# Kernel tuning notes

Measured on AMD Instinct MI355X. Metric: run time of the kernel, lower is better.

## Reference

```python
import jax, jax.numpy as jnp
import numpy as np

BS, SEQ, NPL = 1024, 200, 22
HID = 128          # hidden_dim / rnn_dim
RNN_H = 2 * HID    # LSTMCell hidden = 256
ENC_D = HID // 2   # per-team set-encoder output = 64
IN_D = 2 * ENC_D + 44 + 3  # 175 = coords_encoded(128) + flat player trace(44) + closest_dist(1) + prev pred(2)
OUT_D = 2 + 88     # 'ball' target


def setup_inputs() -> dict:
    key = jax.random.key(0)
    ks = jax.random.split(key, 8)
    s = jnp.float32(0.02)
    return {
        "coords": jax.random.uniform(ks[0], (BS, SEQ, NPL * 4), dtype=jnp.float32),
        "pitch_size": jnp.ones((2,), jnp.float32),
        "W_e1": jax.random.normal(ks[1], (2, ENC_D), jnp.float32) * s,
        "b_e1": jnp.zeros((ENC_D,), jnp.float32),
        "W_e2": jax.random.normal(ks[2], (ENC_D, ENC_D), jnp.float32) * s,
        "b_e2": jnp.zeros((ENC_D,), jnp.float32),
        "W_ih": jax.random.normal(ks[3], (IN_D, 4 * RNN_H), jnp.float32) * s,
        "b_ih": jnp.zeros((4 * RNN_H,), jnp.float32),
        "W_hh": jax.random.normal(ks[4], (RNN_H, 4 * RNN_H), jnp.float32) * s,
        "b_hh": jnp.zeros((4 * RNN_H,), jnp.float32),
        "W_out": jax.random.normal(ks[5], (RNN_H, OUT_D), jnp.float32) * s,
        "b_out": jnp.zeros((OUT_D,), jnp.float32),
    }


def reference(coords, pitch_size, W_e1, b_e1, W_e2, b_e2,
              W_ih, b_ih, W_hh, b_hh, W_out, b_out):
    bs, seq_len, _ = coords.shape

    # per-team set encoder (DeepSets stand-in for SetTransformer(in=2, out=rnn_dim//2))
    pts = coords.reshape(bs, seq_len, NPL, 4)[..., :2]          # [bs, seq, 22, 2]
    def enc(t):                                                 # [bs, seq, 11, 2] -> [bs, seq, 64]
        h = jax.nn.relu(t @ W_e1 + b_e1)
        return h.mean(axis=2) @ W_e2 + b_e2
    coords_enc = jnp.concatenate(
        [enc(pts[:, :, :NPL // 2]), enc(pts[:, :, NPL // 2:])], axis=-1)  # [bs, seq, 128]

    # strided gathers: player_x = coords[..., 0:88:4], player_y = coords[..., 1:88:4]
    ptrace = jnp.stack([coords[:, :, 0:88:4], coords[:, :, 1:88:4]], axis=-1)  # [bs, seq, 22, 2]

    scale = jnp.tile(pitch_size, 45)                            # pitch_size.repeat(45) -> [90]

    def step(carry, xs):
        hx, cx, pred = carry                                    # pred = previous step_out[:, -2:]
        ptr_t, enc_t = xs                                       # [bs,22,2], [bs,128]
        dists = jnp.linalg.norm(pred[:, None, :] - ptr_t, axis=-1)   # [bs, 22]
        closest = jnp.min(dists, axis=-1, keepdims=True)             # [bs, 1]
        rnn_in = jnp.concatenate(
            [ptr_t.reshape(bs, -1), enc_t, closest, pred], axis=-1)  # [bs, 175]
        gates = rnn_in @ W_ih + b_ih + hx @ W_hh + b_hh              # [bs, 1024]
        i, f, g, o = jnp.split(gates, 4, axis=-1)
        cx2 = jax.nn.sigmoid(f) * cx + jax.nn.sigmoid(i) * jnp.tanh(g)
        hx2 = jax.nn.sigmoid(o) * jnp.tanh(cx2)
        step_out = (hx2 @ W_out + b_out) * scale                     # [bs, 90]
        return (hx2, cx2, step_out[:, -2:]), step_out

    init = (jnp.zeros((bs, RNN_H), coords.dtype),
            jnp.zeros((bs, RNN_H), coords.dtype),
            jnp.zeros((bs, 2), coords.dtype))
    xs = (ptrace.transpose(1, 0, 2, 3), coords_enc.transpose(1, 0, 2))
    _, outs = jax.lax.scan(step, init, xs)                      # [seq, bs, 90]
    return outs.transpose(1, 0, 2)                              # [bs, seq, 90]
```

## Files before the change

### kernel.cpp

```cpp
#include <hip/hip_runtime.h>
#include <math.h>

#define SEQ 200

typedef float f32x4 __attribute__((ext_vector_type(4)));
typedef short bf16x8 __attribute__((ext_vector_type(8)));

__device__ __forceinline__ float sigmoidf_(float x) { return 1.0f / (1.0f + __expf(-x)); }

__device__ __forceinline__ unsigned short bf16_rn(float v) {
    unsigned x = __float_as_uint(v);
    unsigned r = x + 0x7FFFu + ((x >> 16) & 1u);
    return (unsigned short)(r >> 16);
}
__device__ __forceinline__ float bf16_to_f(unsigned short h) {
    return __uint_as_float(((unsigned)h) << 16);
}
__device__ __forceinline__ void cvt_hl(float v, unsigned short& h, unsigned short& l) {
    h = bf16_rn(v);
    l = bf16_rn(v - bf16_to_f(h));
}

__global__ void prep_wt(const float* __restrict__ W_ih, const float* __restrict__ W_hh,
                        unsigned short* __restrict__ Wt_h, unsigned short* __restrict__ Wt_l) {
    int rc = blockIdx.x;
    int hj = rc >> 7, lc = rc & 127;
    int gcol = (lc >> 5) * 256 + hj * 32 + (lc & 31);
    for (int k = threadIdx.x; k < 448; k += 256) {
        float v = 0.f;
        if (k < 175) v = W_ih[(size_t)k * 1024 + gcol];
        else if (k >= 176 && k < 432) v = W_hh[(size_t)(k - 176) * 1024 + gcol];
        unsigned short h, l; cvt_hl(v, h, l);
        Wt_h[(size_t)rc * 448 + k] = h;
        Wt_l[(size_t)rc * 448 + k] = l;
    }
}

__global__ void prep_wo(const float* __restrict__ W_out,
                        unsigned short* __restrict__ Wt_oh, unsigned short* __restrict__ Wt_ol) {
    int rc = blockIdx.x;
    int hj = rc >> 4, c = rc & 15;
    int col = (c < 12) ? (hj * 12 + c) : (c < 14 ? 76 + c : 999);
    for (int k = threadIdx.x; k < 256; k += 256) {
        float v = (col < 90) ? W_out[(size_t)k * 90 + col] : 0.f;
        unsigned short h, l; cvt_hl(v, h, l);
        Wt_oh[(size_t)rc * 256 + k] = h;
        Wt_ol[(size_t)rc * 256 + k] = l;
    }
}

__global__ __launch_bounds__(256, 3) void enc_kernel(
    const float* __restrict__ coords,
    const float* __restrict__ W_e1, const float* __restrict__ b_e1,
    const float* __restrict__ W_e2, const float* __restrict__ b_e2,
    unsigned short* __restrict__ xin_h)
{
    __shared__ float C[32][45];
    __shared__ float H[32][2][65];
    __shared__ float W2[64][64];
    __shared__ unsigned short O16[128][34];

    int t  = blockIdx.x >> 5;
    int bc = blockIdx.x & 31;
    int tid = threadIdx.x;

    for (int idx = tid; idx < 32 * 44; idx += 256) {
        int bl = idx / 44, j = idx - bl * 44;
        C[bl][j] = coords[((size_t)(bc * 32 + bl) * SEQ + t) * 88 + (j >> 1) * 4 + (j & 1)];
    }
    for (int idx = tid; idx < 64 * 64; idx += 256)
        W2[idx >> 6][idx & 63] = W_e2[idx];
    __syncthreads();

    {
        int b  = tid >> 3;
        int cq = (tid & 7) * 8;
        float w0[8], w1[8], bb[8];
#pragma unroll
        for (int c = 0; c < 8; c++) { w0[c] = W_e1[cq + c]; w1[c] = W_e1[64 + cq + c]; bb[c] = b_e1[cq + c]; }
        for (int tm = 0; tm < 2; tm++) {
            float acc[8];
#pragma unroll
            for (int c = 0; c < 8; c++) acc[c] = 0.f;
            for (int p = 0; p < 11; p++) {
                float x = C[b][tm * 22 + p * 2];
                float y = C[b][tm * 22 + p * 2 + 1];
#pragma unroll
                for (int c = 0; c < 8; c++) {
                    float h = fmaf(x, w0[c], fmaf(y, w1[c], bb[c]));
                    acc[c] += fmaxf(h, 0.f);
                }
            }
#pragma unroll
            for (int c = 0; c < 8; c++) H[b][tm][cq + c] = acc[c] * (1.0f / 11.0f);
        }
    }
    __syncthreads();

    {
        int b  = tid >> 3;
        int tm = (tid >> 2) & 1;
        int ch = (tid & 3) * 16;
        float acc[16];
#pragma unroll
        for (int c = 0; c < 16; c++) acc[c] = 0.f;
        for (int k = 0; k < 64; k++) {
            float h = H[b][tm][k];
#pragma unroll
            for (int c = 0; c < 16; c++) acc[c] = fmaf(h, W2[k][ch + c], acc[c]);
        }
#pragma unroll
        for (int c = 0; c < 16; c++)
            O16[tm * 64 + ch + c][b] = bf16_rn(acc[c] + b_e2[ch + c]);
    }
    __syncthreads();

    unsigned short* xrow = xin_h + ((size_t)t * 1024 + bc * 32) * 176;
    for (int idx = tid; idx < 32 * 22; idx += 256) {
        int bl = idx / 22, oct = idx - bl * 22;
        unsigned short hs[8];
#pragma unroll
        for (int e = 0; e < 8; e++) {
            int k = oct * 8 + e;
            if (k < 44)       hs[e] = bf16_rn(C[bl][k]);
            else if (k < 172) hs[e] = O16[k - 44][bl];
            else              hs[e] = 0;
        }
        uint4 pk;
        pk.x = (unsigned)hs[0] | ((unsigned)hs[1] << 16);
        pk.y = (unsigned)hs[2] | ((unsigned)hs[3] << 16);
        pk.z = (unsigned)hs[4] | ((unsigned)hs[5] << 16);
        pk.w = (unsigned)hs[6] | ((unsigned)hs[7] << 16);
        *(uint4*)(xrow + (size_t)bl * 176 + oct * 8) = pk;
    }
}

#define MFMA_B(d, a, b) d = __builtin_amdgcn_mfma_f32_16x16x32_bf16(a, b, d, 0, 0, 0)

#define P_LOAD(R0, R1, R2, R3, KO) \
    R0 = *(const uint4*)(wbh + (size_t)c0 * 448 + (KO) + oct * 8); \
    R1 = *(const uint4*)(wbl + (size_t)c0 * 448 + (KO) + oct * 8); \
    R2 = *(const uint4*)(wbh + (size_t)c1 * 448 + (KO) + oct * 8); \
    R3 = *(const uint4*)(wbl + (size_t)c1 * 448 + (KO) + oct * 8);

#define P_STORE(R0, R1, R2, R3, NB) \
    *(uint4*)&BB[NB][0][c0 * 40 + oct * 8] = R0; \
    *(uint4*)&BB[NB][1][c0 * 40 + oct * 8] = R1; \
    *(uint4*)&BB[NB][0][c1 * 40 + oct * 8] = R2; \
    *(uint4*)&BB[NB][1][c1 * 40 + oct * 8] = R3;

__global__ __launch_bounds__(512, 1) void step_kernel(
    int t,
    const unsigned short* __restrict__ xin_h,
    const unsigned short* __restrict__ hxh_in, const unsigned short* __restrict__ hxl_in,
    unsigned short* __restrict__ hxh_out, unsigned short* __restrict__ hxl_out,
    float* __restrict__ cx,
    const unsigned short* __restrict__ Wt_h, const unsigned short* __restrict__ Wt_l,
    const unsigned short* __restrict__ Wt_oh, const unsigned short* __restrict__ Wt_ol,
    const float* __restrict__ b_ih, const float* __restrict__ b_hh,
    const float* __restrict__ b_out,
    const float* __restrict__ pitch, float* __restrict__ d_out)
{
    __shared__ unsigned short AH[32 * 456];
    __shared__ unsigned short AL[32 * 456];
    __shared__ unsigned short BB[3][2][128 * 40];
    __shared__ float U[128 * 33];
    __shared__ float predL[32][2];

    int tid = threadIdx.x;
    int bi = blockIdx.x & 31, hj = blockIdx.x >> 5;
    int bg0 = bi * 32;
    int l = tid & 63, w = (tid >> 6) & 3;
    int lr = l & 15, qa = l >> 4;

    const unsigned short* wbh = Wt_h + (size_t)(hj * 128) * 448;
    const unsigned short* wbl = Wt_l + (size_t)(hj * 128) * 448;

    for (int idx = tid; idx < 32 * 32; idx += 512) {
        int b = idx >> 5, oct = idx & 31;
        *(uint4*)&AH[b * 456 + 176 + oct * 8] =
            *(const uint4*)(hxh_in + (size_t)(bg0 + b) * 256 + oct * 8);
        *(uint4*)&AL[b * 456 + 176 + oct * 8] =
            *(const uint4*)(hxl_in + (size_t)(bg0 + b) * 256 + oct * 8);
    }
    if (t < SEQ) {
        const unsigned short* xr = xin_h + ((size_t)t * 1024 + bg0) * 176;
        for (int idx = tid; idx < 32 * 22; idx += 512) {
            int b = idx / 22, oct = idx - b * 22;
            *(uint4*)&AH[b * 456 + oct * 8] = *(const uint4*)(xr + (size_t)b * 176 + oct * 8);
        }
        if (tid < 64) {
            int b = tid >> 1, h8 = (tid & 1) * 8;
            *(uint4*)&AL[b * 456 + 160 + h8] = make_uint4(0, 0, 0, 0);
            *(uint4*)&AH[b * 456 + 432 + h8] = make_uint4(0, 0, 0, 0);
            *(uint4*)&AL[b * 456 + 432 + h8] = make_uint4(0, 0, 0, 0);
        }
        {
            int c = tid >> 2, o = tid & 3;
            *(uint4*)&BB[0][0][c * 40 + o * 8] = *(const uint4*)(wbh + (size_t)c * 448 + o * 8);
            *(uint4*)&BB[0][1][c * 40 + o * 8] = *(const uint4*)(wbl + (size_t)c * 448 + o * 8);
        }
    }
    __syncthreads();

    uint4 rA0, rA1, rA2, rA3, rB0, rB1, rB2, rB3;
    int c0 = (tid & 255) >> 2, oct = tid & 3, c1 = ((tid & 255) >> 2) + 64;
    if (tid < 256) {
        const unsigned short* woh = Wt_oh + ((size_t)(hj * 16 + lr)) * 256 + w * 64 + qa * 8;
        const unsigned short* wol = Wt_ol + ((size_t)(hj * 16 + lr)) * 256 + w * 64 + qa * 8;
        bf16x8 bh0 = *(const bf16x8*)(woh);
        bf16x8 bl0 = *(const bf16x8*)(wol);
        bf16x8 bh1 = *(const bf16x8*)(woh + 32);
        bf16x8 bl1 = *(const bf16x8*)(wol + 32);
        f32x4 acce[2];
        acce[0] = (f32x4){0.f, 0.f, 0.f, 0.f};
        acce[1] = (f32x4){0.f, 0.f, 0.f, 0.f};
#pragma unroll
        for (int ks2 = 0; ks2 < 2; ks2++) {
            bf16x8 bh = ks2 ? bh1 : bh0;
            bf16x8 bl = ks2 ? bl1 : bl0;
#pragma unroll
            for (int mt = 0; mt < 2; mt++) {
                bf16x8 ah = *(const bf16x8*)&AH[(mt * 16 + lr) * 456 + 176 + w * 64 + ks2 * 32 + qa * 8];
                bf16x8 al = *(const bf16x8*)&AL[(mt * 16 + lr) * 456 + 176 + w * 64 + ks2 * 32 + qa * 8];
                MFMA_B(acce[mt], ah, bh);
                MFMA_B(acce[mt], ah, bl);
                MFMA_B(acce[mt], al, bh);
            }
        }
#pragma unroll
        for (int mt = 0; mt < 2; mt++)
#pragma unroll
            for (int r = 0; r < 4; r++)
                U[w * 512 + (mt * 16 + qa * 4 + r) * 16 + lr] = acce[mt][r];
    } else if (t < SEQ) {
        P_LOAD(rA0, rA1, rA2, rA3, 32)
        P_LOAD(rB0, rB1, rB2, rB3, 64)
    }
    __syncthreads();

    if (tid < 256) {
#pragma unroll
        for (int j = 0; j < 2; j++) {
            int i = tid * 2 + j;
            int b = i >> 4, c = i & 15;
            float v = U[i] + U[512 + i] + U[1024 + i] + U[1536 + i];
            if (c < 14) {
                int col = (c < 12) ? (hj * 12 + c) : (76 + c);
                if (col < 90) {
                    if (t > 0) {
                        float vv = (v + b_out[col]) * pitch[c & 1];
                        if (c < 12) d_out[((size_t)(bg0 + b) * SEQ + (t - 1)) * 90 + col] = vv;
                        else predL[b][c - 12] = vv;
                    } else if (c >= 12) {
                        predL[b][c - 12] = 0.f;
                    }
                }
            }
        }
    }
    __syncthreads();

    if (t < SEQ) {
        if (tid < 32) {
            int b = tid;
            float p0 = predL[b][0], p1 = predL[b][1];
            float m = 1e30f;
#pragma unroll
            for (int p = 0; p < 22; p++) {
                float px = bf16_to_f(AH[b * 456 + 2 * p]);
                float py = bf16_to_f(AH[b * 456 + 2 * p + 1]);
                float dx = p0 - px, dy = p1 - py;
                m = fminf(m, fmaf(dx, dx, dy * dy));
            }
            unsigned short h, lo;
            cvt_hl(sqrtf(m), h, lo); AH[b * 456 + 172] = h; AL[b * 456 + 172] = lo;
            cvt_hl(p0, h, lo);       AH[b * 456 + 173] = h; AL[b * 456 + 173] = lo;
            cvt_hl(p1, h, lo);       AH[b * 456 + 174] = h; AL[b * 456 + 174] = lo;
        }
        __syncthreads();

        if (tid < 256) {
            f32x4 acc[2][2];
#pragma unroll
            for (int ct = 0; ct < 2; ct++)
#pragma unroll
                for (int mt = 0; mt < 2; mt++) acc[ct][mt] = (f32x4){0.f, 0.f, 0.f, 0.f};

#pragma unroll
            for (int ks = 0; ks < 14; ks++) {
                const int cur = ks % 3;
                bf16x8 ah[2], al[2], bh[2], bl[2];
#pragma unroll
                for (int mt = 0; mt < 2; mt++)
                    ah[mt] = *(const bf16x8*)&AH[(mt * 16 + lr) * 456 + ks * 32 + qa * 8];
                if (ks >= 5) {
#pragma unroll
                    for (int mt = 0; mt < 2; mt++)
                        al[mt] = *(const bf16x8*)&AL[(mt * 16 + lr) * 456 + ks * 32 + qa * 8];
                }
#pragma unroll
                for (int ct = 0; ct < 2; ct++) {
                    bh[ct] = *(const bf16x8*)&BB[cur][0][(w * 32 + ct * 16 + lr) * 40 + qa * 8];
                    bl[ct] = *(const bf16x8*)&BB[cur][1][(w * 32 + ct * 16 + lr) * 40 + qa * 8];
                }
#pragma unroll
                for (int ct = 0; ct < 2; ct++)
#pragma unroll
                    for (int mt = 0; mt < 2; mt++) {
                        MFMA_B(acc[ct][mt], ah[mt], bh[ct]);
                        MFMA_B(acc[ct][mt], ah[mt], bl[ct]);
                        if (ks >= 5) MFMA_B(acc[ct][mt], al[mt], bh[ct]);
                    }
                __syncthreads();
            }

#pragma unroll
            for (int ct = 0; ct < 2; ct++)
#pragma unroll
                for (int mt = 0; mt < 2; mt++)
#pragma unroll
                    for (int r = 0; r < 4; r++)
                        U[(w * 32 + ct * 16 + lr) * 33 + (mt * 16 + qa * 4 + r)] = acc[ct][mt][r];
        } else {
#pragma unroll
            for (int ks = 0; ks < 14; ks++) {
                if (ks <= 12) {
                    const int nb = (ks + 1) % 3;
                    if ((ks & 1) == 0) { P_STORE(rA0, rA1, rA2, rA3, nb) }
                    else               { P_STORE(rB0, rB1, rB2, rB3, nb) }
                }
                if (ks <= 10) {
                    const int ko = (ks + 3) * 32;
                    if ((ks & 1) == 0) { P_LOAD(rA0, rA1, rA2, rA3, ko) }
                    else               { P_LOAD(rB0, rB1, rB2, rB3, ko) }
                }
                __syncthreads();
            }
        }
        __syncthreads();

        if (tid < 256) {
            int b = tid & 31, hq = tid >> 5;
            unsigned short hh[4], hl[4];
#pragma unroll
            for (int q = 0; q < 4; q++) {
                int hlc = hq * 4 + q;
                int gb = hj * 32 + hlc;
                float iv = U[(0 * 32 + hlc) * 33 + b] + b_ih[gb]        + b_hh[gb];
                float fv = U[(1 * 32 + hlc) * 33 + b] + b_ih[256 + gb]  + b_hh[256 + gb];
                float gv = U[(2 * 32 + hlc) * 33 + b] + b_ih[512 + gb]  + b_hh[512 + gb];
                float ov = U[(3 * 32 + hlc) * 33 + b] + b_ih[768 + gb]  + b_hh[768 + gb];
                size_t cidx = (size_t)gb * 1024 + bg0 + b;
                float c_old = cx[cidx];
                float c_new = fmaf(sigmoidf_(fv), c_old, sigmoidf_(iv) * tanhf(gv));
                cx[cidx] = c_new;
                float hv = sigmoidf_(ov) * tanhf(c_new);
                cvt_hl(hv, hh[q], hl[q]);
            }
            size_t ho = (size_t)(bg0 + b) * 256 + hj * 32 + hq * 4;
            *(ushort4*)&hxh_out[ho] = make_ushort4(hh[0], hh[1], hh[2], hh[3]);
            *(ushort4*)&hxl_out[ho] = make_ushort4(hl[0], hl[1], hl[2], hl[3]);
        }
    }
}

extern "C" void kernel_launch(void* const* d_in, const int* in_sizes, int n_in,
                              void* d_out, int out_size, void* d_ws, size_t ws_size,
                              hipStream_t stream) {
    const float* coords = (const float*)d_in[0];
    const float* pitch  = (const float*)d_in[1];
    const float* W_e1   = (const float*)d_in[2];
    const float* b_e1   = (const float*)d_in[3];
    const float* W_e2   = (const float*)d_in[4];
    const float* b_e2   = (const float*)d_in[5];
    const float* W_ih   = (const float*)d_in[6];
    const float* b_ih   = (const float*)d_in[7];
    const float* W_hh   = (const float*)d_in[8];
    const float* b_hh   = (const float*)d_in[9];
    const float* W_out  = (const float*)d_in[10];
    const float* b_out  = (const float*)d_in[11];
    float* out = (float*)d_out;
    float* ws  = (float*)d_ws;

    float* cxb = ws;
    unsigned short* hxhA = (unsigned short*)(ws + 262144);
    unsigned short* hxlA = (unsigned short*)(ws + 393216);
    unsigned short* hxhB = (unsigned short*)(ws + 524288);
    unsigned short* hxlB = (unsigned short*)(ws + 655360);
    unsigned short* Wt_h = (unsigned short*)(ws + 786432);
    unsigned short* Wt_l = (unsigned short*)(ws + 1015808);
    unsigned short* Wt_oh = (unsigned short*)(ws + 1245184);
    unsigned short* Wt_ol = (unsigned short*)(ws + 1261568);
    unsigned short* xin_h = (unsigned short*)(ws + 1277952);

    hipMemsetAsync(ws, 0, (size_t)524288 * sizeof(float), stream);

    prep_wt<<<1024, 256, 0, stream>>>(W_ih, W_hh, Wt_h, Wt_l);
    prep_wo<<<128, 256, 0, stream>>>(W_out, Wt_oh, Wt_ol);
    enc_kernel<<<SEQ * 32, 256, 0, stream>>>(coords, W_e1, b_e1, W_e2, b_e2, xin_h);

    for (int t = 0; t <= SEQ; t++) {
        bool even = !(t & 1);
        step_kernel<<<256, 512, 0, stream>>>(
            t, xin_h,
            even ? hxhA : hxhB, even ? hxlA : hxlB,
            even ? hxhB : hxhA, even ? hxlB : hxlA,
            cxb, Wt_h, Wt_l, Wt_oh, Wt_ol, b_ih, b_hh, b_out, pitch, out);
    }
}
```

Baseline: 2.380 ms.

## Split step kernel into 512 smaller blocks reading weights directly from global

Each step block now covers 16 hidden units (64 gate columns) instead of 32, so the grid doubles to 512 blocks of 256 threads and every thread does MFMA work. The producer/consumer LDS triple-buffering of weight tiles is removed; MFMA B operands are loaded straight from global memory, relying on L2/cache. The output projection split is adjusted to 6 columns per block. This trades the LDS weight pipeline and the extra synchronisation it needed for more parallelism across the GPU's compute units. The cost is more redundant loading of the A (input/hidden) tile across blocks and global-latency-bound B loads.

New measurement: 2.800 ms. 1.18x slower.

```diff
diff --git a/kernel.cpp b/kernel.cpp
--- a/kernel.cpp
+++ b/kernel.cpp
@@ -24,8 +24,8 @@
 __global__ void prep_wt(const float* __restrict__ W_ih, const float* __restrict__ W_hh,
                         unsigned short* __restrict__ Wt_h, unsigned short* __restrict__ Wt_l) {
     int rc = blockIdx.x;
-    int hj = rc >> 7, lc = rc & 127;
-    int gcol = (lc >> 5) * 256 + hj * 32 + (lc & 31);
+    int hj = rc >> 6, lc = rc & 63;
+    int gcol = (lc >> 4) * 256 + hj * 16 + (lc & 15);
     for (int k = threadIdx.x; k < 448; k += 256) {
         float v = 0.f;
         if (k < 175) v = W_ih[(size_t)k * 1024 + gcol];
@@ -40,7 +40,7 @@
                         unsigned short* __restrict__ Wt_oh, unsigned short* __restrict__ Wt_ol) {
     int rc = blockIdx.x;
     int hj = rc >> 4, c = rc & 15;
-    int col = (c < 12) ? (hj * 12 + c) : (c < 14 ? 76 + c : 999);
+    int col = (c < 6) ? (hj * 6 + c) : (c < 8 ? 82 + c : 999);
     for (int k = threadIdx.x; k < 256; k += 256) {
         float v = (col < 90) ? W_out[(size_t)k * 90 + col] : 0.f;
         unsigned short h, l; cvt_hl(v, h, l);
@@ -137,19 +137,7 @@
 
 #define MFMA_B(d, a, b) d = __builtin_amdgcn_mfma_f32_16x16x32_bf16(a, b, d, 0, 0, 0)
 
-#define P_LOAD(R0, R1, R2, R3, KO) \
-    R0 = *(const uint4*)(wbh + (size_t)c0 * 448 + (KO) + oct * 8); \
-    R1 = *(const uint4*)(wbl + (size_t)c0 * 448 + (KO) + oct * 8); \
-    R2 = *(const uint4*)(wbh + (size_t)c1 * 448 + (KO) + oct * 8); \
-    R3 = *(const uint4*)(wbl + (size_t)c1 * 448 + (KO) + oct * 8);
-
-#define P_STORE(R0, R1, R2, R3, NB) \
-    *(uint4*)&BB[NB][0][c0 * 40 + oct * 8] = R0; \
-    *(uint4*)&BB[NB][1][c0 * 40 + oct * 8] = R1; \
-    *(uint4*)&BB[NB][0][c1 * 40 + oct * 8] = R2; \
-    *(uint4*)&BB[NB][1][c1 * 40 + oct * 8] = R3;
-
-__global__ __launch_bounds__(512, 1) void step_kernel(
+__global__ __launch_bounds__(256, 2) void step_kernel(
     int t,
     const unsigned short* __restrict__ xin_h,
     const unsigned short* __restrict__ hxh_in, const unsigned short* __restrict__ hxl_in,
@@ -163,20 +151,19 @@
 {
     __shared__ unsigned short AH[32 * 456];
     __shared__ unsigned short AL[32 * 456];
-    __shared__ unsigned short BB[3][2][128 * 40];
-    __shared__ float U[128 * 33];
+    __shared__ float U[2112];
     __shared__ float predL[32][2];
 
     int tid = threadIdx.x;
     int bi = blockIdx.x & 31, hj = blockIdx.x >> 5;
     int bg0 = bi * 32;
-    int l = tid & 63, w = (tid >> 6) & 3;
+    int l = tid & 63, w = tid >> 6;
     int lr = l & 15, qa = l >> 4;
 
-    const unsigned short* wbh = Wt_h + (size_t)(hj * 128) * 448;
-    const unsigned short* wbl = Wt_l + (size_t)(hj * 128) * 448;
-
-    for (int idx = tid; idx < 32 * 32; idx += 512) {
+    const unsigned short* wbh = Wt_h + (size_t)(hj * 64) * 448;
+    const unsigned short* wbl = Wt_l + (size_t)(hj * 64) * 448;
+
+    for (int idx = tid; idx < 32 * 32; idx += 256) {
         int b = idx >> 5, oct = idx & 31;
         *(uint4*)&AH[b * 456 + 176 + oct * 8] =
             *(const uint4*)(hxh_in + (size_t)(bg0 + b) * 256 + oct * 8);
@@ -185,7 +172,7 @@
     }
     if (t < SEQ) {
         const unsigned short* xr = xin_h + ((size_t)t * 1024 + bg0) * 176;
-        for (int idx = tid; idx < 32 * 22; idx += 512) {
+        for (int idx = tid; idx < 32 * 22; idx += 256) {
             int b = idx / 22, oct = idx - b * 22;
             *(uint4*)&AH[b * 456 + oct * 8] = *(const uint4*)(xr + (size_t)b * 176 + oct * 8);
         }
@@ -195,17 +182,10 @@
             *(uint4*)&AH[b * 456 + 432 + h8] = make_uint4(0, 0, 0, 0);
             *(uint4*)&AL[b * 456 + 432 + h8] = make_uint4(0, 0, 0, 0);
         }
-        {
-            int c = tid >> 2, o = tid & 3;
-            *(uint4*)&BB[0][0][c * 40 + o * 8] = *(const uint4*)(wbh + (size_t)c * 448 + o * 8);
-            *(uint4*)&BB[0][1][c * 40 + o * 8] = *(const uint4*)(wbl + (size_t)c * 448 + o * 8);
-        }
-    }
-    __syncthreads();
-
-    uint4 rA0, rA1, rA2, rA3, rB0, rB1, rB2, rB3;
-    int c0 = (tid & 255) >> 2, oct = tid & 3, c1 = ((tid & 255) >> 2) + 64;
-    if (tid < 256) {
+    }
+    __syncthreads();
+
+    {
         const unsigned short* woh = Wt_oh + ((size_t)(hj * 16 + lr)) * 256 + w * 64 + qa * 8;
         const unsigned short* wol = Wt_ol + ((size_t)(hj * 16 + lr)) * 256 + w * 64 + qa * 8;
         bf16x8 bh0 = *(const bf16x8*)(woh);
@@ -233,28 +213,21 @@
 #pragma unroll
             for (int r = 0; r < 4; r++)
                 U[w * 512 + (mt * 16 + qa * 4 + r) * 16 + lr] = acce[mt][r];
-    } else if (t < SEQ) {
-        P_LOAD(rA0, rA1, rA2, rA3, 32)
-        P_LOAD(rB0, rB1, rB2, rB3, 64)
-    }
-    __syncthreads();
-
-    if (tid < 256) {
-#pragma unroll
-        for (int j = 0; j < 2; j++) {
-            int i = tid * 2 + j;
-            int b = i >> 4, c = i & 15;
-            float v = U[i] + U[512 + i] + U[1024 + i] + U[1536 + i];
-            if (c < 14) {
-                int col = (c < 12) ? (hj * 12 + c) : (76 + c);
-                if (col < 90) {
-                    if (t > 0) {
-                        float vv = (v + b_out[col]) * pitch[c & 1];
-                        if (c < 12) d_out[((size_t)(bg0 + b) * SEQ + (t - 1)) * 90 + col] = vv;
-                        else predL[b][c - 12] = vv;
-                    } else if (c >= 12) {
-                        predL[b][c - 12] = 0.f;
-                    }
+    }
+    __syncthreads();
+
+    for (int idx = tid; idx < 512; idx += 256) {
+        int b = idx >> 4, c = idx & 15;
+        float v = U[idx] + U[512 + idx] + U[1024 + idx] + U[1536 + idx];
+        if (c < 8) {
+            int col = (c < 6) ? (hj * 6 + c) : (82 + c);
+            if (col < 90) {
+                if (t > 0) {
+                    float vv = (v + b_out[col]) * pitch[c & 1];
+                    if (c < 6) d_out[((size_t)(bg0 + b) * SEQ + (t - 1)) * 90 + col] = vv;
+                    else predL[b][c - 6] = vv;
+                } else if (c >= 6) {
+                    predL[b][c - 6] = 0.f;
                 }
             }
         }
@@ -280,87 +253,56 @@
         }
         __syncthreads();
 
-        if (tid < 256) {
-            f32x4 acc[2][2];
-#pragma unroll
-            for (int ct = 0; ct < 2; ct++)
-#pragma unroll
-                for (int mt = 0; mt < 2; mt++) acc[ct][mt] = (f32x4){0.f, 0.f, 0.f, 0.f};
-
+        {
+            f32x4 acc[2];
+            acc[0] = (f32x4){0.f, 0.f, 0.f, 0.f};
+            acc[1] = (f32x4){0.f, 0.f, 0.f, 0.f};
 #pragma unroll
             for (int ks = 0; ks < 14; ks++) {
-                const int cur = ks % 3;
-                bf16x8 ah[2], al[2], bh[2], bl[2];
-#pragma unroll
-                for (int mt = 0; mt < 2; mt++)
-                    ah[mt] = *(const bf16x8*)&AH[(mt * 16 + lr) * 456 + ks * 32 + qa * 8];
+                bf16x8 ah0 = *(const bf16x8*)&AH[(lr) * 456 + ks * 32 + qa * 8];
+                bf16x8 ah1 = *(const bf16x8*)&AH[(16 + lr) * 456 + ks * 32 + qa * 8];
+                bf16x8 bh = *(const bf16x8*)(wbh + (size_t)(w * 16 + lr) * 448 + ks * 32 + qa * 8);
+                bf16x8 bl = *(const bf16x8*)(wbl + (size_t)(w * 16 + lr) * 448 + ks * 32 + qa * 8);
+                MFMA_B(acc[0], ah0, bh);
+                MFMA_B(acc[0], ah0, bl);
+                MFMA_B(acc[1], ah1, bh);
+                MFMA_B(acc[1], ah1, bl);
                 if (ks >= 5) {
-#pragma unroll
-                    for (int mt = 0; mt < 2; mt++)
-                        al[mt] = *(const bf16x8*)&AL[(mt * 16 + lr) * 456 + ks * 32 + qa * 8];
+                    bf16x8 al0 = *(const bf16x8*)&AL[(lr) * 456 + ks * 32 + qa * 8];
+                    bf16x8 al1 = *(const bf16x8*)&AL[(16 + lr) * 456 + ks * 32 + qa * 8];
+                    MFMA_B(acc[0], al0, bh);
+                    MFMA_B(acc[1], al1, bh);
                 }
-#pragma unroll
-                for (int ct = 0; ct < 2; ct++) {
-                    bh[ct] = *(const bf16x8*)&BB[cur][0][(w * 32 + ct * 16 + lr) * 40 + qa * 8];
-                    bl[ct] = *(const bf16x8*)&BB[cur][1][(w * 32 + ct * 16 + lr) * 40 + qa * 8];
-                }
-#pragma unroll
-                for (int ct = 0; ct < 2; ct++)
-#pragma unroll
-                    for (int mt = 0; mt < 2; mt++) {
-                        MFMA_B(acc[ct][mt], ah[mt], bh[ct]);
-                        MFMA_B(acc[ct][mt], ah[mt], bl[ct]);
-                        if (ks >= 5) MFMA_B(acc[ct][mt], al[mt], bh[ct]);
-                    }
-                __syncthreads();
-            }
-
-#pragma unroll
-            for (int ct = 0; ct < 2; ct++)
-#pragma unroll
-                for (int mt = 0; mt < 2; mt++)
-#pragma unroll
-                    for (int r = 0; r < 4; r++)
-                        U[(w * 32 + ct * 16 + lr) * 33 + (mt * 16 + qa * 4 + r)] = acc[ct][mt][r];
-        } else {
-#pragma unroll
-            for (int ks = 0; ks < 14; ks++) {
-                if (ks <= 12) {
-                    const int nb = (ks + 1) % 3;
-                    if ((ks & 1) == 0) { P_STORE(rA0, rA1, rA2, rA3, nb) }
-                    else               { P_STORE(rB0, rB1, rB2, rB3, nb) }
-                }
-                if (ks <= 10) {
-                    const int ko = (ks + 3) * 32;
-                    if ((ks & 1) == 0) { P_LOAD(rA0, rA1, rA2, rA3, ko) }
-                    else               { P_LOAD(rB0, rB1, rB2, rB3, ko) }
-                }
-                __syncthreads();
-            }
+            }
+#pragma unroll
+            for (int mt = 0; mt < 2; mt++)
+#pragma unroll
+                for (int r = 0; r < 4; r++)
+                    U[(w * 16 + lr) * 33 + (mt * 16 + qa * 4 + r)] = acc[mt][r];
         }
         __syncthreads();
 
-        if (tid < 256) {
+        {
             int b = tid & 31, hq = tid >> 5;
-            unsigned short hh[4], hl[4];
-#pragma unroll
-            for (int q = 0; q < 4; q++) {
-                int hlc = hq * 4 + q;
-                int gb = hj * 32 + hlc;
-                float iv = U[(0 * 32 + hlc) * 33 + b] + b_ih[gb]        + b_hh[gb];
-                float fv = U[(1 * 32 + hlc) * 33 + b] + b_ih[256 + gb]  + b_hh[256 + gb];
-                float gv = U[(2 * 32 + hlc) * 33 + b] + b_ih[512 + gb]  + b_hh[512 + gb];
-                float ov = U[(3 * 32 + hlc) * 33 + b] + b_ih[768 + gb]  + b_hh[768 + gb];
+            unsigned short hh2[2], hl2[2];
+#pragma unroll
+            for (int q = 0; q < 2; q++) {
+                int hlc = hq * 2 + q;
+                int gb = hj * 16 + hlc;
+                float iv = U[(0 * 16 + hlc) * 33 + b] + b_ih[gb]        + b_hh[gb];
+                float fv = U[(1 * 16 + hlc) * 33 + b] + b_ih[256 + gb]  + b_hh[256 + gb];
+                float gv = U[(2 * 16 + hlc) * 33 + b] + b_ih[512 + gb]  + b_hh[512 + gb];
+                float ov = U[(3 * 16 + hlc) * 33 + b] + b_ih[768 + gb]  + b_hh[768 + gb];
                 size_t cidx = (size_t)gb * 1024 + bg0 + b;
                 float c_old = cx[cidx];
                 float c_new = fmaf(sigmoidf_(fv), c_old, sigmoidf_(iv) * tanhf(gv));
                 cx[cidx] = c_new;
                 float hv = sigmoidf_(ov) * tanhf(c_new);
-                cvt_hl(hv, hh[q], hl[q]);
-            }
-            size_t ho = (size_t)(bg0 + b) * 256 + hj * 32 + hq * 4;
-            *(ushort4*)&hxh_out[ho] = make_ushort4(hh[0], hh[1], hh[2], hh[3]);
-            *(ushort4*)&hxl_out[ho] = make_ushort4(hl[0], hl[1], hl[2], hl[3]);
+                cvt_hl(hv, hh2[q], hl2[q]);
+            }
+            size_t ho = (size_t)(bg0 + b) * 256 + hj * 16 + hq * 2;
+            *(ushort2*)&hxh_out[ho] = make_ushort2(hh2[0], hh2[1]);
+            *(ushort2*)&hxl_out[ho] = make_ushort2(hl2[0], hl2[1]);
         }
     }
 }
@@ -391,18 +333,18 @@
     unsigned short* Wt_h = (unsigned short*)(ws + 786432);
     unsigned short* Wt_l = (unsigned short*)(ws + 1015808);
     unsigned short* Wt_oh = (unsigned short*)(ws + 1245184);
-    unsigned short* Wt_ol = (unsigned short*)(ws + 1261568);
-    unsigned short* xin_h = (unsigned short*)(ws + 1277952);
+    unsigned short* Wt_ol = (unsigned short*)(ws + 1277952);
+    unsigned short* xin_h = (unsigned short*)(ws + 1310720);
 
     hipMemsetAsync(ws, 0, (size_t)524288 * sizeof(float), stream);
 
     prep_wt<<<1024, 256, 0, stream>>>(W_ih, W_hh, Wt_h, Wt_l);
-    prep_wo<<<128, 256, 0, stream>>>(W_out, Wt_oh, Wt_ol);
+    prep_wo<<<256, 256, 0, stream>>>(W_out, Wt_oh, Wt_ol);
     enc_kernel<<<SEQ * 32, 256, 0, stream>>>(coords, W_e1, b_e1, W_e2, b_e2, xin_h);
 
     for (int t = 0; t <= SEQ; t++) {
         bool even = !(t & 1);
-        step_kernel<<<256, 512, 0, stream>>>(
+        step_kernel<<<512, 256, 0, stream>>>(
             t, xin_h,
             even ? hxhA : hxhB, even ? hxlA : hxlB,
             even ? hxhB : hxhA, even ? hxlB : hxlA,
```
